# Kernel tuning notes

Hardware: AMD Instinct MI355X
Metric: run time of the kernel (lower is better)

## Reference

```python
import jax, jax.numpy as jnp
import numpy as np

POS_SCALE = 50.0
LEN_SCALE = 500.0

N_NODES = 100000
N_EDGES = 600000
IN_DIM = 128
HID_DIM = 128


def setup_inputs() -> dict:
    key = jax.random.key(0)
    ks = jax.random.split(key, 12)
    x = jax.random.normal(ks[0], (N_NODES, IN_DIM), dtype=jnp.float32)
    positions = jax.random.randint(ks[1], (N_NODES,), 0, 50, dtype=jnp.int64)
    lengths = jax.random.randint(ks[2], (N_NODES,), 0, 500, dtype=jnp.int64)
    edge_index = jax.random.randint(ks[3], (2, N_EDGES), 0, N_NODES, dtype=jnp.int64)
    reranker_scores = jax.random.normal(ks[4], (N_NODES,), dtype=jnp.float32)
    s = 1.0 / np.sqrt(IN_DIM + 2)
    fp_w = jax.random.uniform(ks[5], (IN_DIM + 2, IN_DIM), minval=-s, maxval=s, dtype=jnp.float32)
    fp_b = jnp.zeros((IN_DIM,), jnp.float32)
    s2 = 1.0 / np.sqrt(IN_DIM)
    lin_l_w = jax.random.uniform(ks[6], (IN_DIM, HID_DIM), minval=-s2, maxval=s2, dtype=jnp.float32)
    lin_l_b = jnp.zeros((HID_DIM,), jnp.float32)
    lin_r_w = jax.random.uniform(ks[7], (IN_DIM, HID_DIM), minval=-s2, maxval=s2, dtype=jnp.float32)
    res_w = jax.random.uniform(ks[8], (IN_DIM, HID_DIM), minval=-s2, maxval=s2, dtype=jnp.float32)
    res_b = jnp.zeros((HID_DIM,), jnp.float32)
    s3 = 1.0 / np.sqrt(HID_DIM)
    sh_w = jax.random.uniform(ks[9], (HID_DIM, 1), minval=-s3, maxval=s3, dtype=jnp.float32)
    sh_b = jnp.zeros((1,), jnp.float32)
    alpha = jnp.asarray(0.65, jnp.float32)
    return {
        "x": x, "positions": positions, "lengths": lengths,
        "edge_index": edge_index, "reranker_scores": reranker_scores,
        "fp_w": fp_w, "fp_b": fp_b,
        "lin_l_w": lin_l_w, "lin_l_b": lin_l_b, "lin_r_w": lin_r_w,
        "res_w": res_w, "res_b": res_b,
        "sh_w": sh_w, "sh_b": sh_b, "alpha": alpha,
    }


def reference(x, positions, lengths, edge_index, reranker_scores,
              fp_w, fp_b, lin_l_w, lin_l_b, lin_r_w, res_w, res_b,
              sh_w, sh_b, alpha):
    n = x.shape[0]
    # position/length features
    pos_feat = positions[:, None].astype(x.dtype) / POS_SCALE
    len_feat = lengths[:, None].astype(x.dtype) / LEN_SCALE
    xf = jnp.concatenate([x, pos_feat, len_feat], axis=-1)  # [N, D+2]
    xf = xf @ fp_w + fp_b                                   # [N, D]
    h_in = xf @ res_w + res_b                               # residual proj [N, H]
    # SAGEConv with mean aggregation: out = lin_l(mean_{j->i} x_j) + lin_r(x_i)
    src, dst = edge_index[0], edge_index[1]
    msg_sum = jax.ops.segment_sum(xf[src], dst, num_segments=n)          # [N, D]
    cnt = jax.ops.segment_sum(jnp.ones((src.shape[0], 1), xf.dtype), dst, num_segments=n)
    agg = msg_sum / jnp.maximum(cnt, 1.0)
    h = jax.nn.relu(agg @ lin_l_w + lin_l_b + xf @ lin_r_w)  # [N, H]
    # dropout is identity in eval mode
    h = h + h_in
    gnn_scores = (h @ sh_w + sh_b)[:, 0]                     # [N]
    a = jax.nn.sigmoid(alpha)
    return a * reranker_scores + (1.0 - a) * gnn_scores
```

## Files before the change

kernel.cpp:

```cpp
#include <hip/hip_runtime.h>
#include <hip/hip_bf16.h>
#include <cstdint>

#define D 128
#define LDSPITCH 136
#define CAP 32

typedef __attribute__((ext_vector_type(4))) float f32x4;
typedef __attribute__((ext_vector_type(8))) short s16x8;

__device__ __forceinline__ unsigned short f2b(float f) {
    union { float f; uint32_t u; } v; v.f = f;
    uint32_t b = v.u + 0x7fffu + ((v.u >> 16) & 1u);
    return (unsigned short)(b >> 16);
}
__device__ __forceinline__ float b2f(unsigned short u) {
    union { uint32_t u; float f; } v; v.u = ((uint32_t)u) << 16; return v.f;
}

__global__ __launch_bounds__(256) void k_prep(
    const float* __restrict__ fp_w, const float* __restrict__ lin_l_w,
    const float* __restrict__ lin_r_w,
    unsigned short* __restrict__ Btf, unsigned short* __restrict__ Btl,
    unsigned short* __restrict__ Btr,
    const float* __restrict__ res_w, const float* __restrict__ res_b,
    const float* __restrict__ sh_w, const float* __restrict__ sh_b,
    const float* __restrict__ alpha, float* __restrict__ c1, float* __restrict__ scal,
    int* __restrict__ cursor, int N) {
    int bid = blockIdx.x, tid = threadIdx.x;
    if (bid < 192) {
        int m = bid >> 6;
        int i = (bid & 63) * 256 + tid;
        const float* src = (m == 0) ? fp_w : (m == 1) ? lin_l_w : lin_r_w;
        unsigned short* dst = (m == 0) ? Btf : (m == 1) ? Btl : Btr;
        int k = i >> 7, n = i & 127;
        dst[n * D + k] = f2b(src[k * D + n]);
    } else if (bid == 192) {
        if (tid < 128) {
            float s = 0.f;
            for (int j = 0; j < D; ++j) s += res_w[tid * D + j] * sh_w[j];
            c1[tid] = s;
            if (tid == 0) {
                float c0 = 0.f;
                for (int j = 0; j < D; ++j) c0 += res_b[j] * sh_w[j];
                c0 += sh_b[0];
                float a = 1.f / (1.f + expf(-alpha[0]));
                scal[0] = a; scal[1] = c0;
            }
        }
    } else {
        int i = ((bid - 193) * 256 + tid) * 4;
        if (i < N) {
            if (i + 3 < N) *(int4*)(cursor + i) = (int4){0, 0, 0, 0};
            else { for (int k = i; k < N; ++k) cursor[k] = 0; }
        }
    }
}

__global__ __launch_bounds__(256) void k_gemm1(
    const float* __restrict__ x, unsigned short* __restrict__ xb,
    const int* __restrict__ positions, const int* __restrict__ lengths,
    const unsigned short* __restrict__ Btf,
    const float* __restrict__ fp_w, const float* __restrict__ fp_b,
    const float* __restrict__ c1, float* __restrict__ d1, int N, int mb,
    const int* __restrict__ ei, int* __restrict__ cursor, int* __restrict__ srcs, int E) {
    if (blockIdx.x >= mb) {
        int e = (blockIdx.x - mb) * 256 + threadIdx.x;
        if (e < E) {
            int src = ei[e];
            int dst = ei[E + e];
            int pos = atomicAdd(&cursor[dst], 1);
            if (pos < CAP) srcs[dst * CAP + pos] = src;
        }
        return;
    }
    int lane = threadIdx.x & 63;
    int wv = threadIdx.x >> 6;
    int col = lane & 15, q = lane >> 4;
    int row0 = blockIdx.x * 64 + wv * 16;
    int arow = row0 + col; if (arow > N - 1) arow = N - 1;

    f32x4 acc[8];
#pragma unroll
    for (int nt = 0; nt < 8; ++nt) acc[nt] = (f32x4){0.f, 0.f, 0.f, 0.f};

#pragma unroll
    for (int ks = 0; ks < 4; ++ks) {
        const float* xp = x + (size_t)arow * D + ks * 32 + q * 8;
        float4 a0 = *(const float4*)xp;
        float4 a1 = *(const float4*)(xp + 4);
        s16x8 af;
        af[0] = (short)f2b(a0.x); af[1] = (short)f2b(a0.y);
        af[2] = (short)f2b(a0.z); af[3] = (short)f2b(a0.w);
        af[4] = (short)f2b(a1.x); af[5] = (short)f2b(a1.y);
        af[6] = (short)f2b(a1.z); af[7] = (short)f2b(a1.w);
#pragma unroll
        for (int nt = 0; nt < 8; ++nt) {
            s16x8 bf = *(const s16x8*)(Btf + (size_t)(nt * 16 + col) * D + ks * 32 + q * 8);
            acc[nt] = __builtin_amdgcn_mfma_f32_16x16x32_bf16(af, bf, acc[nt], 0, 0, 0);
        }
    }

    float pf[4], lf[4];
#pragma unroll
    for (int r = 0; r < 4; ++r) {
        int rr = row0 + q * 4 + r; int rc = rr < N ? rr : N - 1;
        pf[r] = (float)positions[rc] * (1.0f / 50.0f);
        lf[r] = (float)lengths[rc] * (1.0f / 500.0f);
    }
    float sdot[4] = {0.f, 0.f, 0.f, 0.f};
#pragma unroll
    for (int nt = 0; nt < 8; ++nt) {
        int n = nt * 16 + col;
        float bias = fp_b[n];
        float w128 = fp_w[128 * D + n];
        float w129 = fp_w[129 * D + n];
        float c1v = c1[n];
#pragma unroll
        for (int r = 0; r < 4; ++r) {
            float t = acc[nt][r] + bias + pf[r] * w128 + lf[r] * w129;
            int rr = row0 + q * 4 + r;
            if (rr < N) xb[(size_t)rr * D + n] = f2b(t);
            sdot[r] += t * c1v;
        }
    }
#pragma unroll
    for (int r = 0; r < 4; ++r) {
        float s = sdot[r];
        s += __shfl_xor(s, 1, 64);
        s += __shfl_xor(s, 2, 64);
        s += __shfl_xor(s, 4, 64);
        s += __shfl_xor(s, 8, 64);
        if (col == 0) {
            int rr = row0 + q * 4 + r;
            if (rr < N) d1[rr] = s;
        }
    }
}

__global__ __launch_bounds__(256) void k_gemm2(
    const unsigned short* __restrict__ xfb,
    const int* __restrict__ cursor, const int* __restrict__ srcs,
    const unsigned short* __restrict__ Btl, const unsigned short* __restrict__ Btr,
    const float* __restrict__ lin_l_b, const float* __restrict__ sh_w,
    const float* __restrict__ rer, const float* __restrict__ d1,
    const float* __restrict__ scal, float* __restrict__ out, int N) {
    __shared__ unsigned short agg[64 * LDSPITCH];
    int lane = threadIdx.x & 63;
    int wv = threadIdx.x >> 6;
    int li = lane & 15, q = lane >> 4;
    int wrow0 = blockIdx.x * 64 + wv * 16;
    int Nm1 = N - 1;

    int rowc[4];
#pragma unroll
    for (int rr = 0; rr < 4; ++rr) {
        int row = wrow0 + rr * 4 + q;
        rowc[rr] = row < Nm1 ? row : Nm1;
    }
    int4 ia[4], ib[4];
    int deg[4];
#pragma unroll
    for (int rr = 0; rr < 4; ++rr) {
        const int* sp = srcs + (size_t)rowc[rr] * CAP;
        ia[rr] = *(const int4*)sp;
        ib[rr] = *(const int4*)(sp + 4);
        deg[rr] = cursor[rowc[rr]];
    }
    int arow = wrow0 + li; if (arow > Nm1) arow = Nm1;
    s16x8 afx[4];
#pragma unroll
    for (int ks = 0; ks < 4; ++ks)
        afx[ks] = *(const s16x8*)(xfb + (size_t)arow * D + ks * 32 + q * 8);

    float t[4][8];
#pragma unroll
    for (int rr = 0; rr < 4; ++rr)
#pragma unroll
        for (int k2 = 0; k2 < 8; ++k2) t[rr][k2] = 0.f;

#pragma unroll
    for (int rr = 0; rr < 4; ++rr) {
        int dg = deg[rr] > CAP ? CAP : deg[rr];
        int ix[8] = {ia[rr].x, ia[rr].y, ia[rr].z, ia[rr].w,
                     ib[rr].x, ib[rr].y, ib[rr].z, ib[rr].w};
        s16x8 v[8];
#pragma unroll
        for (int k = 0; k < 8; ++k) {
            int c = ix[k];
            c = c > 0 ? c : 0;
            c = c < Nm1 ? c : Nm1;
            v[k] = *(const s16x8*)(xfb + (size_t)c * D + li * 8);
        }
        float w[8];
#pragma unroll
        for (int k = 0; k < 8; ++k) w[k] = (k < dg) ? 1.f : 0.f;
#pragma unroll
        for (int k = 0; k < 8; ++k)
#pragma unroll
            for (int k2 = 0; k2 < 8; ++k2)
                t[rr][k2] += w[k] * b2f((unsigned short)v[k][k2]);
    }

#pragma unroll
    for (int rr = 0; rr < 4; ++rr) {
        int dg = deg[rr] > CAP ? CAP : deg[rr];
        if (dg > 8) {
            const int* sp = srcs + (size_t)rowc[rr] * CAP;
            for (int j = 8; j < dg; j += 8) {
                int4 ic = *(const int4*)(sp + j);
                int4 id = *(const int4*)(sp + j + 4);
                int ix[8] = {ic.x, ic.y, ic.z, ic.w, id.x, id.y, id.z, id.w};
                s16x8 v[8];
#pragma unroll
                for (int k = 0; k < 8; ++k) {
                    int c = ix[k];
                    c = c > 0 ? c : 0;
                    c = c < Nm1 ? c : Nm1;
                    v[k] = *(const s16x8*)(xfb + (size_t)c * D + li * 8);
                }
                float w[8];
#pragma unroll
                for (int k = 0; k < 8; ++k) w[k] = (j + k < dg) ? 1.f : 0.f;
#pragma unroll
                for (int k = 0; k < 8; ++k)
#pragma unroll
                    for (int k2 = 0; k2 < 8; ++k2)
                        t[rr][k2] += w[k] * b2f((unsigned short)v[k][k2]);
            }
        }
    }

#pragma unroll
    for (int rr = 0; rr < 4; ++rr) {
        int dg = deg[rr] > CAP ? CAP : deg[rr];
        float rc = 1.0f / (float)(dg > 0 ? dg : 1);
        s16x8 o;
#pragma unroll
        for (int k2 = 0; k2 < 8; ++k2) o[k2] = (short)f2b(t[rr][k2] * rc);
        *(s16x8*)(agg + (wv * 16 + rr * 4 + q) * LDSPITCH + li * 8) = o;
    }

    f32x4 acc[8];
#pragma unroll
    for (int nt = 0; nt < 8; ++nt) acc[nt] = (f32x4){0.f, 0.f, 0.f, 0.f};

#pragma unroll
    for (int ks = 0; ks < 4; ++ks) {
        s16x8 afa = *(const s16x8*)(agg + (wv * 16 + li) * LDSPITCH + ks * 32 + q * 8);
        s16x8 bfl[8];
#pragma unroll
        for (int nt = 0; nt < 8; ++nt)
            bfl[nt] = *(const s16x8*)(Btl + (size_t)(nt * 16 + li) * D + ks * 32 + q * 8);
#pragma unroll
        for (int nt = 0; nt < 8; ++nt)
            acc[nt] = __builtin_amdgcn_mfma_f32_16x16x32_bf16(afa, bfl[nt], acc[nt], 0, 0, 0);
        s16x8 bfr[8];
#pragma unroll
        for (int nt = 0; nt < 8; ++nt)
            bfr[nt] = *(const s16x8*)(Btr + (size_t)(nt * 16 + li) * D + ks * 32 + q * 8);
#pragma unroll
        for (int nt = 0; nt < 8; ++nt)
            acc[nt] = __builtin_amdgcn_mfma_f32_16x16x32_bf16(afx[ks], bfr[nt], acc[nt], 0, 0, 0);
    }

    float a = scal[0], c0 = scal[1];
    float sdot[4] = {0.f, 0.f, 0.f, 0.f};
#pragma unroll
    for (int nt = 0; nt < 8; ++nt) {
        int n = nt * 16 + li;
        float bias = lin_l_b[n];
        float shw = sh_w[n];
#pragma unroll
        for (int r = 0; r < 4; ++r) {
            float tt = acc[nt][r] + bias;
            sdot[r] += fmaxf(tt, 0.f) * shw;
        }
    }
#pragma unroll
    for (int r = 0; r < 4; ++r) {
        float s = sdot[r];
        s += __shfl_xor(s, 1, 64);
        s += __shfl_xor(s, 2, 64);
        s += __shfl_xor(s, 4, 64);
        s += __shfl_xor(s, 8, 64);
        if (li == 0) {
            int rr = wrow0 + q * 4 + r;
            if (rr < N) out[rr] = a * rer[rr] + (1.f - a) * (c0 + d1[rr] + s);
        }
    }
}

extern "C" void kernel_launch(void* const* d_in, const int* in_sizes, int n_in,
                              void* d_out, int out_size, void* d_ws, size_t ws_size,
                              hipStream_t stream) {
    const float* x        = (const float*)d_in[0];
    const int*   positions= (const int*)d_in[1];
    const int*   lengths  = (const int*)d_in[2];
    const int*   ei       = (const int*)d_in[3];
    const float* rer      = (const float*)d_in[4];
    const float* fp_w     = (const float*)d_in[5];
    const float* fp_b     = (const float*)d_in[6];
    const float* lin_l_w  = (const float*)d_in[7];
    const float* lin_l_b  = (const float*)d_in[8];
    const float* lin_r_w  = (const float*)d_in[9];
    const float* res_w    = (const float*)d_in[10];
    const float* res_b    = (const float*)d_in[11];
    const float* sh_w     = (const float*)d_in[12];
    const float* sh_b     = (const float*)d_in[13];
    const float* alpha    = (const float*)d_in[14];
    int N = in_sizes[1];
    int E = in_sizes[3] / 2;
    float* out = (float*)d_out;

    char* ws = (char*)d_ws;
    size_t off = 0;
    auto alloc = [&](size_t bytes) -> void* {
        void* p = ws + off;
        off = (off + bytes + 255) & ~(size_t)255;
        return p;
    };
    unsigned short* xb  = (unsigned short*)alloc((size_t)N * D * 2);
    int* srcs    = (int*)alloc((size_t)N * CAP * 4);
    int* cursor  = (int*)alloc((size_t)N * 4);
    float* d1    = (float*)alloc((size_t)N * 4);
    unsigned short* Btf = (unsigned short*)alloc(D * D * 2);
    unsigned short* Btl = (unsigned short*)alloc(D * D * 2);
    unsigned short* Btr = (unsigned short*)alloc(D * D * 2);
    float* c1    = (float*)alloc(D * 4);
    float* scal  = (float*)alloc(16);

    int mb = (N + 63) / 64;
    int cb = (E + 255) / 256;
    int zb = (N + 1023) / 1024;

    k_prep<<<193 + zb, 256, 0, stream>>>(fp_w, lin_l_w, lin_r_w, Btf, Btl, Btr,
                                         res_w, res_b, sh_w, sh_b, alpha, c1, scal,
                                         cursor, N);
    k_gemm1<<<mb + cb, 256, 0, stream>>>(x, xb, positions, lengths, Btf, fp_w, fp_b,
                                         c1, d1, N, mb, ei, cursor, srcs, E);
    k_gemm2<<<mb, 256, 0, stream>>>(xb, cursor, srcs, Btl, Btr, lin_l_b, sh_w, rer, d1, scal, out, N);
}
```

Measured before the change: 250.7 us.

## Split neighbor gather out of fused GEMM into separate kernel

Moves the mean-aggregation gather out of the fused gather+GEMM kernel into its own kernel. The new kernel assigns one row per 16 threads and writes the bf16 aggregate to a global buffer, which a slimmer GEMM kernel then reads. The aim is higher occupancy and more memory parallelism for the irregular gather, which had been limited by the GEMM kernel's register and LDS use. The cost is an extra kernel launch and a round trip of an N×128 bf16 buffer through global memory.

Result: slower. 262.1 us (+4.6%).

```diff
diff --git a/kernel.cpp b/kernel.cpp
--- a/kernel.cpp
+++ b/kernel.cpp
@@ -3,7 +3,6 @@
 #include <cstdint>
 
 #define D 128
-#define LDSPITCH 136
 #define CAP 32
 
 typedef __attribute__((ext_vector_type(4))) float f32x4;
@@ -138,107 +137,94 @@
     }
 }
 
-__global__ __launch_bounds__(256) void k_gemm2(
+__global__ __launch_bounds__(256) void k_gather(
     const unsigned short* __restrict__ xfb,
     const int* __restrict__ cursor, const int* __restrict__ srcs,
+    unsigned short* __restrict__ aggb, int N) {
+    int li = threadIdx.x & 15;
+    int row = (int)((blockIdx.x * 256 + threadIdx.x) >> 4);
+    if (row >= N) return;
+    int Nm1 = N - 1;
+
+    const int* sp = srcs + (size_t)row * CAP;
+    int4 ia = *(const int4*)sp;
+    int4 ib = *(const int4*)(sp + 4);
+    int deg = cursor[row];
+    int dg = deg > CAP ? CAP : deg;
+
+    float t[8];
+#pragma unroll
+    for (int k2 = 0; k2 < 8; ++k2) t[k2] = 0.f;
+
+    {
+        int ix[8] = {ia.x, ia.y, ia.z, ia.w, ib.x, ib.y, ib.z, ib.w};
+        s16x8 v[8];
+#pragma unroll
+        for (int k = 0; k < 8; ++k) {
+            int c = ix[k];
+            c = c > 0 ? c : 0;
+            c = c < Nm1 ? c : Nm1;
+            v[k] = *(const s16x8*)(xfb + (size_t)c * D + li * 8);
+        }
+        float w[8];
+#pragma unroll
+        for (int k = 0; k < 8; ++k) w[k] = (k < dg) ? 1.f : 0.f;
+#pragma unroll
+        for (int k = 0; k < 8; ++k)
+#pragma unroll
+            for (int k2 = 0; k2 < 8; ++k2)
+                t[k2] += w[k] * b2f((unsigned short)v[k][k2]);
+    }
+
+    if (dg > 8) {
+        for (int j = 8; j < dg; j += 8) {
+            int4 ic = *(const int4*)(sp + j);
+            int4 id = *(const int4*)(sp + j + 4);
+            int ix[8] = {ic.x, ic.y, ic.z, ic.w, id.x, id.y, id.z, id.w};
+            s16x8 v[8];
+#pragma unroll
+            for (int k = 0; k < 8; ++k) {
+                int c = ix[k];
+                c = c > 0 ? c : 0;
+                c = c < Nm1 ? c : Nm1;
+                v[k] = *(const s16x8*)(xfb + (size_t)c * D + li * 8);
+            }
+            float w[8];
+#pragma unroll
+            for (int k = 0; k < 8; ++k) w[k] = (j + k < dg) ? 1.f : 0.f;
+#pragma unroll
+            for (int k = 0; k < 8; ++k)
+#pragma unroll
+                for (int k2 = 0; k2 < 8; ++k2)
+                    t[k2] += w[k] * b2f((unsigned short)v[k][k2]);
+        }
+    }
+
+    float rc = 1.0f / (float)(dg > 0 ? dg : 1);
+    s16x8 o;
+#pragma unroll
+    for (int k2 = 0; k2 < 8; ++k2) o[k2] = (short)f2b(t[k2] * rc);
+    *(s16x8*)(aggb + (size_t)row * D + li * 8) = o;
+}
+
+__global__ __launch_bounds__(256) void k_gemm2d(
+    const unsigned short* __restrict__ xfb, const unsigned short* __restrict__ aggb,
     const unsigned short* __restrict__ Btl, const unsigned short* __restrict__ Btr,
     const float* __restrict__ lin_l_b, const float* __restrict__ sh_w,
     const float* __restrict__ rer, const float* __restrict__ d1,
     const float* __restrict__ scal, float* __restrict__ out, int N) {
-    __shared__ unsigned short agg[64 * LDSPITCH];
     int lane = threadIdx.x & 63;
     int wv = threadIdx.x >> 6;
     int li = lane & 15, q = lane >> 4;
     int wrow0 = blockIdx.x * 64 + wv * 16;
     int Nm1 = N - 1;
-
-    int rowc[4];
-#pragma unroll
-    for (int rr = 0; rr < 4; ++rr) {
-        int row = wrow0 + rr * 4 + q;
-        rowc[rr] = row < Nm1 ? row : Nm1;
-    }
-    int4 ia[4], ib[4];
-    int deg[4];
-#pragma unroll
-    for (int rr = 0; rr < 4; ++rr) {
-        const int* sp = srcs + (size_t)rowc[rr] * CAP;
-        ia[rr] = *(const int4*)sp;
-        ib[rr] = *(const int4*)(sp + 4);
-        deg[rr] = cursor[rowc[rr]];
-    }
     int arow = wrow0 + li; if (arow > Nm1) arow = Nm1;
-    s16x8 afx[4];
-#pragma unroll
-    for (int ks = 0; ks < 4; ++ks)
+
+    s16x8 afa[4], afx[4];
+#pragma unroll
+    for (int ks = 0; ks < 4; ++ks) {
+        afa[ks] = *(const s16x8*)(aggb + (size_t)arow * D + ks * 32 + q * 8);
         afx[ks] = *(const s16x8*)(xfb + (size_t)arow * D + ks * 32 + q * 8);
-
-    float t[4][8];
-#pragma unroll
-    for (int rr = 0; rr < 4; ++rr)
-#pragma unroll
-        for (int k2 = 0; k2 < 8; ++k2) t[rr][k2] = 0.f;
-
-#pragma unroll
-    for (int rr = 0; rr < 4; ++rr) {
-        int dg = deg[rr] > CAP ? CAP : deg[rr];
-        int ix[8] = {ia[rr].x, ia[rr].y, ia[rr].z, ia[rr].w,
-                     ib[rr].x, ib[rr].y, ib[rr].z, ib[rr].w};
-        s16x8 v[8];
-#pragma unroll
-        for (int k = 0; k < 8; ++k) {
-            int c = ix[k];
-            c = c > 0 ? c : 0;
-            c = c < Nm1 ? c : Nm1;
-            v[k] = *(const s16x8*)(xfb + (size_t)c * D + li * 8);
-        }
-        float w[8];
-#pragma unroll
-        for (int k = 0; k < 8; ++k) w[k] = (k < dg) ? 1.f : 0.f;
-#pragma unroll
-        for (int k = 0; k < 8; ++k)
-#pragma unroll
-            for (int k2 = 0; k2 < 8; ++k2)
-                t[rr][k2] += w[k] * b2f((unsigned short)v[k][k2]);
-    }
-
-#pragma unroll
-    for (int rr = 0; rr < 4; ++rr) {
-        int dg = deg[rr] > CAP ? CAP : deg[rr];
-        if (dg > 8) {
-            const int* sp = srcs + (size_t)rowc[rr] * CAP;
-            for (int j = 8; j < dg; j += 8) {
-                int4 ic = *(const int4*)(sp + j);
-                int4 id = *(const int4*)(sp + j + 4);
-                int ix[8] = {ic.x, ic.y, ic.z, ic.w, id.x, id.y, id.z, id.w};
-                s16x8 v[8];
-#pragma unroll
-                for (int k = 0; k < 8; ++k) {
-                    int c = ix[k];
-                    c = c > 0 ? c : 0;
-                    c = c < Nm1 ? c : Nm1;
-                    v[k] = *(const s16x8*)(xfb + (size_t)c * D + li * 8);
-                }
-                float w[8];
-#pragma unroll
-                for (int k = 0; k < 8; ++k) w[k] = (j + k < dg) ? 1.f : 0.f;
-#pragma unroll
-                for (int k = 0; k < 8; ++k)
-#pragma unroll
-                    for (int k2 = 0; k2 < 8; ++k2)
-                        t[rr][k2] += w[k] * b2f((unsigned short)v[k][k2]);
-            }
-        }
-    }
-
-#pragma unroll
-    for (int rr = 0; rr < 4; ++rr) {
-        int dg = deg[rr] > CAP ? CAP : deg[rr];
-        float rc = 1.0f / (float)(dg > 0 ? dg : 1);
-        s16x8 o;
-#pragma unroll
-        for (int k2 = 0; k2 < 8; ++k2) o[k2] = (short)f2b(t[rr][k2] * rc);
-        *(s16x8*)(agg + (wv * 16 + rr * 4 + q) * LDSPITCH + li * 8) = o;
     }
 
     f32x4 acc[8];
@@ -247,14 +233,13 @@
 
 #pragma unroll
     for (int ks = 0; ks < 4; ++ks) {
-        s16x8 afa = *(const s16x8*)(agg + (wv * 16 + li) * LDSPITCH + ks * 32 + q * 8);
         s16x8 bfl[8];
 #pragma unroll
         for (int nt = 0; nt < 8; ++nt)
             bfl[nt] = *(const s16x8*)(Btl + (size_t)(nt * 16 + li) * D + ks * 32 + q * 8);
 #pragma unroll
         for (int nt = 0; nt < 8; ++nt)
-            acc[nt] = __builtin_amdgcn_mfma_f32_16x16x32_bf16(afa, bfl[nt], acc[nt], 0, 0, 0);
+            acc[nt] = __builtin_amdgcn_mfma_f32_16x16x32_bf16(afa[ks], bfl[nt], acc[nt], 0, 0, 0);
         s16x8 bfr[8];
 #pragma unroll
         for (int nt = 0; nt < 8; ++nt)
@@ -321,6 +306,7 @@
         return p;
     };
     unsigned short* xb  = (unsigned short*)alloc((size_t)N * D * 2);
+    unsigned short* aggb= (unsigned short*)alloc((size_t)N * D * 2);
     int* srcs    = (int*)alloc((size_t)N * CAP * 4);
     int* cursor  = (int*)alloc((size_t)N * 4);
     float* d1    = (float*)alloc((size_t)N * 4);
@@ -333,11 +319,13 @@
     int mb = (N + 63) / 64;
     int cb = (E + 255) / 256;
     int zb = (N + 1023) / 1024;
+    int gb = (N + 15) / 16;
 
     k_prep<<<193 + zb, 256, 0, stream>>>(fp_w, lin_l_w, lin_r_w, Btf, Btl, Btr,
                                          res_w, res_b, sh_w, sh_b, alpha, c1, scal,
                                          cursor, N);
     k_gemm1<<<mb + cb, 256, 0, stream>>>(x, xb, positions, lengths, Btf, fp_w, fp_b,
                                          c1, d1, N, mb, ei, cursor, srcs, E);
-    k_gemm2<<<mb, 256, 0, stream>>>(xb, cursor, srcs, Btl, Btr, lin_l_b, sh_w, rer, d1, scal, out, N);
-}
+    k_gather<<<gb, 256, 0, stream>>>(xb, cursor, srcs, aggb, N);
+    k_gemm2d<<<mb, 256, 0, stream>>>(xb, aggb, Btl, Btr, lin_l_b, sh_w, rer, d1, scal, out, N);
+}
```

## Stream neighbor gathers through LDS with async loads and pad degree counters

Applied to the files above, without the earlier changes.

The first-8-neighbor gather in the aggregation kernel now uses global_load_lds into a per-wave LDS staging area. Each row's loads are issued while the previous row is being accumulated, with explicit vmcnt waits setting the pipeline depth. Separately, the per-node degree counters are padded to one per 64-byte stride so that atomic increments on different nodes do not contend on shared cache lines. This costs 16x more counter memory to zero and scattered reads of those counters, and the hand-written waitcnt sequencing is fragile.

Measured after the change: 257.1 us. +2.6%, slower.

```diff
diff --git a/kernel.cpp b/kernel.cpp
--- a/kernel.cpp
+++ b/kernel.cpp
@@ -5,6 +5,7 @@
 #define D 128
 #define LDSPITCH 136
 #define CAP 32
+#define CPAD 16
 
 typedef __attribute__((ext_vector_type(4))) float f32x4;
 typedef __attribute__((ext_vector_type(8))) short s16x8;
@@ -16,6 +17,30 @@
 }
 __device__ __forceinline__ float b2f(unsigned short u) {
     union { uint32_t u; float f; } v; v.u = ((uint32_t)u) << 16; return v.f;
+}
+
+__device__ __forceinline__ void gld16(const void* g, void* l) {
+    __builtin_amdgcn_global_load_lds(
+        (const __attribute__((address_space(1))) void*)g,
+        (__attribute__((address_space(3))) void*)l, 16, 0, 0);
+}
+__device__ __forceinline__ void wait_vm(int n) {
+    switch (n) {
+        case 0: asm volatile("s_waitcnt vmcnt(0)" ::: "memory"); break;
+        case 1: asm volatile("s_waitcnt vmcnt(1)" ::: "memory"); break;
+        case 2: asm volatile("s_waitcnt vmcnt(2)" ::: "memory"); break;
+        case 3: asm volatile("s_waitcnt vmcnt(3)" ::: "memory"); break;
+        case 4: asm volatile("s_waitcnt vmcnt(4)" ::: "memory"); break;
+        case 5: asm volatile("s_waitcnt vmcnt(5)" ::: "memory"); break;
+        case 6: asm volatile("s_waitcnt vmcnt(6)" ::: "memory"); break;
+        default: asm volatile("s_waitcnt vmcnt(7)" ::: "memory"); break;
+    }
+}
+__device__ __forceinline__ int sel8(int4 a, int4 b, int k) {
+    switch (k) {
+        case 0: return a.x; case 1: return a.y; case 2: return a.z; case 3: return a.w;
+        case 4: return b.x; case 5: return b.y; case 6: return b.z; default: return b.w;
+    }
 }
 
 __global__ __launch_bounds__(256) void k_prep(
@@ -26,7 +51,7 @@
     const float* __restrict__ res_w, const float* __restrict__ res_b,
     const float* __restrict__ sh_w, const float* __restrict__ sh_b,
     const float* __restrict__ alpha, float* __restrict__ c1, float* __restrict__ scal,
-    int* __restrict__ cursor, int N) {
+    int* __restrict__ cursor, int NC) {
     int bid = blockIdx.x, tid = threadIdx.x;
     if (bid < 192) {
         int m = bid >> 6;
@@ -50,9 +75,9 @@
         }
     } else {
         int i = ((bid - 193) * 256 + tid) * 4;
-        if (i < N) {
-            if (i + 3 < N) *(int4*)(cursor + i) = (int4){0, 0, 0, 0};
-            else { for (int k = i; k < N; ++k) cursor[k] = 0; }
+        if (i < NC) {
+            if (i + 3 < NC) *(int4*)(cursor + i) = (int4){0, 0, 0, 0};
+            else { for (int k = i; k < NC; ++k) cursor[k] = 0; }
         }
     }
 }
@@ -69,7 +94,7 @@
         if (e < E) {
             int src = ei[e];
             int dst = ei[E + e];
-            int pos = atomicAdd(&cursor[dst], 1);
+            int pos = atomicAdd(&cursor[dst * CPAD], 1);
             if (pos < CAP) srcs[dst * CAP + pos] = src;
         }
         return;
@@ -145,12 +170,13 @@
     const float* __restrict__ lin_l_b, const float* __restrict__ sh_w,
     const float* __restrict__ rer, const float* __restrict__ d1,
     const float* __restrict__ scal, float* __restrict__ out, int N) {
-    __shared__ unsigned short agg[64 * LDSPITCH];
+    __shared__ unsigned char stag[4 * 8192];
     int lane = threadIdx.x & 63;
     int wv = threadIdx.x >> 6;
     int li = lane & 15, q = lane >> 4;
     int wrow0 = blockIdx.x * 64 + wv * 16;
     int Nm1 = N - 1;
+    unsigned char* wbase = stag + wv * 8192;
 
     int rowc[4];
 #pragma unroll
@@ -159,55 +185,51 @@
         rowc[rr] = row < Nm1 ? row : Nm1;
     }
     int4 ia[4], ib[4];
-    int deg[4];
+    int dg[4];
 #pragma unroll
     for (int rr = 0; rr < 4; ++rr) {
         const int* sp = srcs + (size_t)rowc[rr] * CAP;
         ia[rr] = *(const int4*)sp;
         ib[rr] = *(const int4*)(sp + 4);
-        deg[rr] = cursor[rowc[rr]];
-    }
-    int arow = wrow0 + li; if (arow > Nm1) arow = Nm1;
-    s16x8 afx[4];
-#pragma unroll
-    for (int ks = 0; ks < 4; ++ks)
-        afx[ks] = *(const s16x8*)(xfb + (size_t)arow * D + ks * 32 + q * 8);
+        dg[rr] = cursor[rowc[rr] * CPAD];
+    }
+#pragma unroll
+    for (int rr = 0; rr < 4; ++rr) dg[rr] = dg[rr] > CAP ? CAP : dg[rr];
 
     float t[4][8];
 #pragma unroll
     for (int rr = 0; rr < 4; ++rr)
 #pragma unroll
-        for (int k2 = 0; k2 < 8; ++k2) t[rr][k2] = 0.f;
-
-#pragma unroll
-    for (int rr = 0; rr < 4; ++rr) {
-        int dg = deg[rr] > CAP ? CAP : deg[rr];
-        int ix[8] = {ia[rr].x, ia[rr].y, ia[rr].z, ia[rr].w,
-                     ib[rr].x, ib[rr].y, ib[rr].z, ib[rr].w};
-        s16x8 v[8];
+        for (int c = 0; c < 8; ++c) t[rr][c] = 0.f;
+
+#pragma unroll
+    for (int k = 0; k < 8; ++k) {
+        int c = sel8(ia[0], ib[0], k);
+        c = c > 0 ? c : 0; c = c < Nm1 ? c : Nm1;
+        gld16(xfb + (size_t)c * D + li * 8, wbase + k * 1024);
+    }
+#pragma unroll
+    for (int rr = 0; rr < 4; ++rr) {
 #pragma unroll
         for (int k = 0; k < 8; ++k) {
-            int c = ix[k];
-            c = c > 0 ? c : 0;
-            c = c < Nm1 ? c : Nm1;
-            v[k] = *(const s16x8*)(xfb + (size_t)c * D + li * 8);
-        }
-        float w[8];
-#pragma unroll
-        for (int k = 0; k < 8; ++k) w[k] = (k < dg) ? 1.f : 0.f;
-#pragma unroll
-        for (int k = 0; k < 8; ++k)
-#pragma unroll
-            for (int k2 = 0; k2 < 8; ++k2)
-                t[rr][k2] += w[k] * b2f((unsigned short)v[k][k2]);
-    }
-
-#pragma unroll
-    for (int rr = 0; rr < 4; ++rr) {
-        int dg = deg[rr] > CAP ? CAP : deg[rr];
-        if (dg > 8) {
+            wait_vm(rr == 3 ? (7 - k) : 7);
+            s16x8 v = *(const s16x8*)(wbase + k * 1024 + lane * 16);
+            float wk = (k < dg[rr]) ? 1.f : 0.f;
+#pragma unroll
+            for (int c = 0; c < 8; ++c) t[rr][c] += wk * b2f((unsigned short)v[c]);
+            if (rr < 3) {
+                int cc = sel8(ia[rr + 1], ib[rr + 1], k);
+                cc = cc > 0 ? cc : 0; cc = cc < Nm1 ? cc : Nm1;
+                gld16(xfb + (size_t)cc * D + li * 8, wbase + k * 1024);
+            }
+        }
+    }
+
+#pragma unroll
+    for (int rr = 0; rr < 4; ++rr) {
+        if (dg[rr] > 8) {
             const int* sp = srcs + (size_t)rowc[rr] * CAP;
-            for (int j = 8; j < dg; j += 8) {
+            for (int j = 8; j < dg[rr]; j += 8) {
                 int4 ic = *(const int4*)(sp + j);
                 int4 id = *(const int4*)(sp + j + 4);
                 int ix[8] = {ic.x, ic.y, ic.z, ic.w, id.x, id.y, id.z, id.w};
@@ -221,25 +243,31 @@
                 }
                 float w[8];
 #pragma unroll
-                for (int k = 0; k < 8; ++k) w[k] = (j + k < dg) ? 1.f : 0.f;
+                for (int k = 0; k < 8; ++k) w[k] = (j + k < dg[rr]) ? 1.f : 0.f;
 #pragma unroll
                 for (int k = 0; k < 8; ++k)
 #pragma unroll
-                    for (int k2 = 0; k2 < 8; ++k2)
-                        t[rr][k2] += w[k] * b2f((unsigned short)v[k][k2]);
+                    for (int c = 0; c < 8; ++c)
+                        t[rr][c] += w[k] * b2f((unsigned short)v[k][c]);
             }
         }
     }
 
-#pragma unroll
-    for (int rr = 0; rr < 4; ++rr) {
-        int dg = deg[rr] > CAP ? CAP : deg[rr];
-        float rc = 1.0f / (float)(dg > 0 ? dg : 1);
+    unsigned short* aggw = (unsigned short*)wbase;
+#pragma unroll
+    for (int rr = 0; rr < 4; ++rr) {
+        float rc = 1.0f / (float)(dg[rr] > 0 ? dg[rr] : 1);
         s16x8 o;
 #pragma unroll
-        for (int k2 = 0; k2 < 8; ++k2) o[k2] = (short)f2b(t[rr][k2] * rc);
-        *(s16x8*)(agg + (wv * 16 + rr * 4 + q) * LDSPITCH + li * 8) = o;
-    }
+        for (int c = 0; c < 8; ++c) o[c] = (short)f2b(t[rr][c] * rc);
+        *(s16x8*)(aggw + (rr * 4 + q) * LDSPITCH + li * 8) = o;
+    }
+
+    int arow = wrow0 + li; if (arow > Nm1) arow = Nm1;
+    s16x8 afx[4];
+#pragma unroll
+    for (int ks = 0; ks < 4; ++ks)
+        afx[ks] = *(const s16x8*)(xfb + (size_t)arow * D + ks * 32 + q * 8);
 
     f32x4 acc[8];
 #pragma unroll
@@ -247,7 +275,7 @@
 
 #pragma unroll
     for (int ks = 0; ks < 4; ++ks) {
-        s16x8 afa = *(const s16x8*)(agg + (wv * 16 + li) * LDSPITCH + ks * 32 + q * 8);
+        s16x8 afa = *(const s16x8*)(aggw + li * LDSPITCH + ks * 32 + q * 8);
         s16x8 bfl[8];
 #pragma unroll
         for (int nt = 0; nt < 8; ++nt)
@@ -322,7 +350,7 @@
     };
     unsigned short* xb  = (unsigned short*)alloc((size_t)N * D * 2);
     int* srcs    = (int*)alloc((size_t)N * CAP * 4);
-    int* cursor  = (int*)alloc((size_t)N * 4);
+    int* cursor  = (int*)alloc((size_t)N * CPAD * 4);
     float* d1    = (float*)alloc((size_t)N * 4);
     unsigned short* Btf = (unsigned short*)alloc(D * D * 2);
     unsigned short* Btl = (unsigned short*)alloc(D * D * 2);
@@ -330,13 +358,14 @@
     float* c1    = (float*)alloc(D * 4);
     float* scal  = (float*)alloc(16);
 
+    int NC = N * CPAD;
     int mb = (N + 63) / 64;
     int cb = (E + 255) / 256;
-    int zb = (N + 1023) / 1024;
+    int zb = (NC / 4 + 255) / 256;
 
     k_prep<<<193 + zb, 256, 0, stream>>>(fp_w, lin_l_w, lin_r_w, Btf, Btl, Btr,
                                          res_w, res_b, sh_w, sh_b, alpha, c1, scal,
-                                         cursor, N);
+                                         cursor, NC);
     k_gemm1<<<mb + cb, 256, 0, stream>>>(x, xb, positions, lengths, Btf, fp_w, fp_b,
                                          c1, d1, N, mb, ei, cursor, srcs, E);
     k_gemm2<<<mb, 256, 0, stream>>>(xb, cursor, srcs, Btl, Btr, lin_l_b, sh_w, rer, d1, scal, out, N);
```

## Replicate edge-bucket counters per XCC and compact neighbor lists in LDS

Applied to the files above, without the earlier changes.

Edge bucketing now keeps separate counters and source slots per XCC (read from the hardware XCC id register) and uses workgroup-scope relaxed atomics. The intent is to keep each atomic inside one XCC's L2 instead of paying for device-scope coherence across dies. The aggregation kernel then merges the eight per-replica lists of each row into a dense LDS array before the gather. In exchange, the workspace grows about fourfold, a larger counter array must be zeroed, and there is an extra LDS compaction step. Correctness also depends on workgroup-scope atomics staying coherent across CUs within one XCC.

Measured after the change: 252.4 us. No clear change (+0.7%).

```diff
diff --git a/kernel.cpp b/kernel.cpp
--- a/kernel.cpp
+++ b/kernel.cpp
@@ -4,7 +4,9 @@
 
 #define D 128
 #define LDSPITCH 136
-#define CAP 32
+#define NREP 8
+#define CAPR 16
+#define DCAP 32
 
 typedef __attribute__((ext_vector_type(4))) float f32x4;
 typedef __attribute__((ext_vector_type(8))) short s16x8;
@@ -26,7 +28,7 @@
     const float* __restrict__ res_w, const float* __restrict__ res_b,
     const float* __restrict__ sh_w, const float* __restrict__ sh_b,
     const float* __restrict__ alpha, float* __restrict__ c1, float* __restrict__ scal,
-    int* __restrict__ cursor, int N) {
+    int* __restrict__ curs, int NC) {
     int bid = blockIdx.x, tid = threadIdx.x;
     if (bid < 192) {
         int m = bid >> 6;
@@ -50,9 +52,9 @@
         }
     } else {
         int i = ((bid - 193) * 256 + tid) * 4;
-        if (i < N) {
-            if (i + 3 < N) *(int4*)(cursor + i) = (int4){0, 0, 0, 0};
-            else { for (int k = i; k < N; ++k) cursor[k] = 0; }
+        if (i < NC) {
+            if (i + 3 < NC) *(int4*)(curs + i) = (int4){0, 0, 0, 0};
+            else { for (int k = i; k < NC; ++k) curs[k] = 0; }
         }
     }
 }
@@ -63,14 +65,19 @@
     const unsigned short* __restrict__ Btf,
     const float* __restrict__ fp_w, const float* __restrict__ fp_b,
     const float* __restrict__ c1, float* __restrict__ d1, int N, int mb,
-    const int* __restrict__ ei, int* __restrict__ cursor, int* __restrict__ srcs, int E) {
+    const int* __restrict__ ei, int* __restrict__ curs, int* __restrict__ srcsR, int E) {
     if (blockIdx.x >= mb) {
         int e = (blockIdx.x - mb) * 256 + threadIdx.x;
         if (e < E) {
+            unsigned xcc;
+            asm volatile("s_getreg_b32 %0, hwreg(HW_REG_XCC_ID)" : "=s"(xcc));
+            int rep = (int)(xcc & (NREP - 1));
             int src = ei[e];
             int dst = ei[E + e];
-            int pos = atomicAdd(&cursor[dst], 1);
-            if (pos < CAP) srcs[dst * CAP + pos] = src;
+            int* ctr = curs + (size_t)dst * NREP + rep;
+            int pos = __hip_atomic_fetch_add(ctr, 1, __ATOMIC_RELAXED,
+                                             __HIP_MEMORY_SCOPE_WORKGROUP);
+            if (pos < CAPR) srcsR[((size_t)dst * NREP + rep) * CAPR + pos] = src;
         }
         return;
     }
@@ -140,50 +147,68 @@
 
 __global__ __launch_bounds__(256) void k_gemm2(
     const unsigned short* __restrict__ xfb,
-    const int* __restrict__ cursor, const int* __restrict__ srcs,
+    const int* __restrict__ curs, const int* __restrict__ srcsR,
     const unsigned short* __restrict__ Btl, const unsigned short* __restrict__ Btr,
     const float* __restrict__ lin_l_b, const float* __restrict__ sh_w,
     const float* __restrict__ rer, const float* __restrict__ d1,
     const float* __restrict__ scal, float* __restrict__ out, int N) {
     __shared__ unsigned short agg[64 * LDSPITCH];
+    __shared__ int dense[64][DCAP];
+    __shared__ int dtot[64];
     int lane = threadIdx.x & 63;
     int wv = threadIdx.x >> 6;
     int li = lane & 15, q = lane >> 4;
     int wrow0 = blockIdx.x * 64 + wv * 16;
     int Nm1 = N - 1;
 
-    int rowc[4];
-#pragma unroll
-    for (int rr = 0; rr < 4; ++rr) {
-        int row = wrow0 + rr * 4 + q;
-        rowc[rr] = row < Nm1 ? row : Nm1;
-    }
-    int4 ia[4], ib[4];
-    int deg[4];
-#pragma unroll
-    for (int rr = 0; rr < 4; ++rr) {
-        const int* sp = srcs + (size_t)rowc[rr] * CAP;
-        ia[rr] = *(const int4*)sp;
-        ib[rr] = *(const int4*)(sp + 4);
-        deg[rr] = cursor[rowc[rr]];
-    }
     int arow = wrow0 + li; if (arow > Nm1) arow = Nm1;
     s16x8 afx[4];
 #pragma unroll
     for (int ks = 0; ks < 4; ++ks)
         afx[ks] = *(const s16x8*)(xfb + (size_t)arow * D + ks * 32 + q * 8);
 
+    {
+        int i16 = lane >> 2, rep4 = lane & 3;
+        int crow = wrow0 + i16; crow = crow < Nm1 ? crow : Nm1;
+        const int* cbp = curs + (size_t)crow * NREP;
+        int4 ca = *(const int4*)cbp;
+        int4 cb = *(const int4*)(cbp + 4);
+        int d[8] = {ca.x, ca.y, ca.z, ca.w, cb.x, cb.y, cb.z, cb.w};
+#pragma unroll
+        for (int r = 0; r < 8; ++r) d[r] = d[r] > CAPR ? CAPR : d[r];
+        int p[8]; int tot = 0;
+#pragma unroll
+        for (int r = 0; r < 8; ++r) { p[r] = tot; tot += d[r]; }
+        if (rep4 == 0) dtot[wv * 16 + i16] = tot > DCAP ? DCAP : tot;
+#pragma unroll
+        for (int h = 0; h < 2; ++h) {
+            int rep = rep4 + h * 4;
+            const int* s = srcsR + ((size_t)crow * NREP + rep) * CAPR;
+            int o = p[rep], dd = d[rep];
+            for (int k = 0; k < dd; ++k) {
+                int o2 = o + k;
+                if (o2 < DCAP) dense[wv * 16 + i16][o2] = s[k];
+            }
+        }
+    }
+
     float t[4][8];
 #pragma unroll
     for (int rr = 0; rr < 4; ++rr)
 #pragma unroll
         for (int k2 = 0; k2 < 8; ++k2) t[rr][k2] = 0.f;
 
+    int degq[4];
+#pragma unroll
+    for (int rr = 0; rr < 4; ++rr) degq[rr] = dtot[wv * 16 + rr * 4 + q];
+
 #pragma unroll
     for (int rr = 0; rr < 4; ++rr) {
-        int dg = deg[rr] > CAP ? CAP : deg[rr];
-        int ix[8] = {ia[rr].x, ia[rr].y, ia[rr].z, ia[rr].w,
-                     ib[rr].x, ib[rr].y, ib[rr].z, ib[rr].w};
+        int dg = degq[rr];
+        const int* dr = &dense[wv * 16 + rr * 4 + q][0];
+        int4 ja = *(const int4*)dr;
+        int4 jb = *(const int4*)(dr + 4);
+        int ix[8] = {ja.x, ja.y, ja.z, ja.w, jb.x, jb.y, jb.z, jb.w};
         s16x8 v[8];
 #pragma unroll
         for (int k = 0; k < 8; ++k) {
@@ -204,13 +229,13 @@
 
 #pragma unroll
     for (int rr = 0; rr < 4; ++rr) {
-        int dg = deg[rr] > CAP ? CAP : deg[rr];
+        int dg = degq[rr];
         if (dg > 8) {
-            const int* sp = srcs + (size_t)rowc[rr] * CAP;
+            const int* dr = &dense[wv * 16 + rr * 4 + q][0];
             for (int j = 8; j < dg; j += 8) {
-                int4 ic = *(const int4*)(sp + j);
-                int4 id = *(const int4*)(sp + j + 4);
-                int ix[8] = {ic.x, ic.y, ic.z, ic.w, id.x, id.y, id.z, id.w};
+                int4 jc = *(const int4*)(dr + j);
+                int4 jd = *(const int4*)(dr + j + 4);
+                int ix[8] = {jc.x, jc.y, jc.z, jc.w, jd.x, jd.y, jd.z, jd.w};
                 s16x8 v[8];
 #pragma unroll
                 for (int k = 0; k < 8; ++k) {
@@ -233,7 +258,7 @@
 
 #pragma unroll
     for (int rr = 0; rr < 4; ++rr) {
-        int dg = deg[rr] > CAP ? CAP : deg[rr];
+        int dg = degq[rr];
         float rc = 1.0f / (float)(dg > 0 ? dg : 1);
         s16x8 o;
 #pragma unroll
@@ -321,8 +346,8 @@
         return p;
     };
     unsigned short* xb  = (unsigned short*)alloc((size_t)N * D * 2);
-    int* srcs    = (int*)alloc((size_t)N * CAP * 4);
-    int* cursor  = (int*)alloc((size_t)N * 4);
+    int* srcsR   = (int*)alloc((size_t)N * NREP * CAPR * 4);
+    int* curs    = (int*)alloc((size_t)N * NREP * 4);
     float* d1    = (float*)alloc((size_t)N * 4);
     unsigned short* Btf = (unsigned short*)alloc(D * D * 2);
     unsigned short* Btl = (unsigned short*)alloc(D * D * 2);
@@ -330,14 +355,15 @@
     float* c1    = (float*)alloc(D * 4);
     float* scal  = (float*)alloc(16);
 
+    int NC = N * NREP;
     int mb = (N + 63) / 64;
     int cb = (E + 255) / 256;
-    int zb = (N + 1023) / 1024;
+    int zb = (NC / 4 + 255) / 256;
 
     k_prep<<<193 + zb, 256, 0, stream>>>(fp_w, lin_l_w, lin_r_w, Btf, Btl, Btr,
                                          res_w, res_b, sh_w, sh_b, alpha, c1, scal,
-                                         cursor, N);
+                                         curs, NC);
     k_gemm1<<<mb + cb, 256, 0, stream>>>(x, xb, positions, lengths, Btf, fp_w, fp_b,
-                                         c1, d1, N, mb, ei, cursor, srcs, E);
-    k_gemm2<<<mb, 256, 0, stream>>>(xb, cursor, srcs, Btl, Btr, lin_l_b, sh_w, rer, d1, scal, out, N);
-}
+                                         c1, d1, N, mb, ei, curs, srcsR, E);
+    k_gemm2<<<mb, 256, 0, stream>>>(xb, curs, srcsR, Btl, Btr, lin_l_b, sh_w, rer, d1, scal, out, N);
+}
```
